# Optimization experiments

Hardware: AMD Instinct MI355X
Metric: run time of the kernel (lower is better)

The kernel has to match this reference:

```python
import jax, jax.numpy as jnp
import numpy as np


def _gru_scan(x, m, d, Wih, Whh, bih, bhh):
    # Returns pre-update hidden at each step (hiddens.append(hidden) BEFORE rnn_cell)
    H = Whh.shape[1]
    B = x.shape[0]
    h0 = jnp.zeros((B, H), x.dtype)
    xs = (jnp.swapaxes(x, 0, 1), jnp.swapaxes(m, 0, 1), jnp.swapaxes(d, 0, 1))  # [T,B,V]

    def step(h, inp):
        xt, mt, dt = inp
        gi = jnp.concatenate([xt, mt, dt], axis=1) @ Wih.T + bih  # [B,3H]
        gh = h @ Whh.T + bhh
        ir, iz, inn = jnp.split(gi, 3, axis=1)
        hr, hz, hn = jnp.split(gh, 3, axis=1)
        r = jax.nn.sigmoid(ir + hr)
        z = jax.nn.sigmoid(iz + hz)
        n = jnp.tanh(inn + r * hn)
        h_new = (1.0 - z) * n + z * h
        return h_new, h

    _, hs = jax.lax.scan(step, h0, xs)
    return jnp.swapaxes(hs, 0, 1)  # [B,T,H]


def setup_inputs() -> dict:
    key = jax.random.key(0)
    B, T, V, H = 512, 128, 59, 512
    ks = jax.random.split(key, 12)

    def u(k, shape, fan_in):
        s = 1.0 / np.sqrt(fan_in).astype(np.float32)
        return jax.random.uniform(k, shape, jnp.float32, -s, s)

    return {
        "values": jax.random.normal(ks[0], (B, T, V), jnp.float32),
        "masks": (jax.random.uniform(ks[1], (B, T, V)) < 0.8).astype(jnp.float32),
        "deltas_f": jax.random.uniform(ks[2], (B, T, V), jnp.float32),
        "deltas_b": jax.random.uniform(ks[3], (B, T, V), jnp.float32),
        # GRUCell(input=3V, hidden=H)
        "Wih": u(ks[4], (3 * H, 3 * V), 3 * V),
        "Whh": u(ks[5], (3 * H, H), H),
        "bih": jnp.zeros((3 * H,), jnp.float32),
        "bhh": jnp.zeros((3 * H,), jnp.float32),
        # hist_reg: Linear(2H -> V)
        "Wh": u(ks[6], (V, 2 * H), 2 * H),
        "bh": jnp.zeros((V,), jnp.float32),
        "Wf": u(ks[7], (V, V), V),
        "bf": jnp.zeros((V,), jnp.float32),
        # weight_combine: Linear(2V -> V)
        "Wc": u(ks[8], (V, 2 * V), 2 * V),
        "bc": jnp.zeros((V,), jnp.float32),
        # imputation: Linear(V -> V)
        "Wi": u(ks[9], (V, V), V),
        "bi": jnp.zeros((V,), jnp.float32),
    }


def reference(values, masks, deltas_f, deltas_b, Wih, Whh, bih, bhh,
              Wh, bh, Wf, bf, Wc, bc, Wi, bi):
    V = values.shape[-1]
    # forward-direction hiddens
    hf = _gru_scan(values, masks, deltas_f, Wih, Whh, bih, bhh)  # [B,T,H]
    # backward-direction: run GRU on time-flipped x/masks with deltas_b, then reverse list
    hb = _gru_scan(values[:, ::-1], masks[:, ::-1], deltas_b, Wih, Whh, bih, bhh)[:, ::-1]
    h = jnp.concatenate([hf, hb], axis=-1)  # [B,T,2H]
    x_v = h @ Wh.T + bh  # hist_reg
    mdiag = 1.0 - jnp.eye(V, dtype=values.dtype)
    x_u = values @ (Wf * mdiag).T + bf  # feat_reg
    x_h = x_u + jnp.concatenate([x_v, masks], axis=-1) @ Wc.T + bc
    imp = x_h @ Wi.T + bi
    # per-timestep masked MAE, summed over T (denominator is per-step mask count)
    num = jnp.sum(jnp.abs(values - imp) * masks, axis=(0, 2))  # [T]
    den = jnp.sum(masks, axis=(0, 2)) + 1e-5
    x_loss = jnp.sum(num / den)
    x_imp = masks * values + (1.0 - masks) * imp
    return x_imp, x_loss
```

## Files before the change

### kernel.cpp

```cpp
#include <hip/hip_runtime.h>
#include <stdint.h>


typedef unsigned short ushort_t;
typedef __bf16 bf16x8 __attribute__((ext_vector_type(8)));
typedef float f32x4 __attribute__((ext_vector_type(4)));
typedef unsigned int u32x4 __attribute__((ext_vector_type(4)));

__device__ __forceinline__ ushort_t f2bf(float f) {
    union { float f; uint32_t u; } c; c.f = f;
    uint32_t u = c.u;
    uint32_t r = (u + 0x7FFFu + ((u >> 16) & 1u)) >> 16;
    return (ushort_t)r;
}

__device__ __forceinline__ u32x4 load_b128_mall(const void* p) {
    u32x4 d;
    asm volatile("global_load_dwordx4 %0, %1, off sc0 sc1"
                 : "=v"(d) : "v"(p) : "memory");
    return d;
}
__device__ __forceinline__ void store_b16_mall(void* p, unsigned v) {
    asm volatile("global_store_short %0, %1, off sc0 sc1"
                 :: "v"(p), "v"(v) : "memory");
}

__device__ __forceinline__ float fast_sigmoid(float x) {
    float e = __expf(-x);
    return __builtin_amdgcn_rcpf(1.f + e);
}
__device__ __forceinline__ float fast_tanh(float x) {
    float xc = fminf(fmaxf(x, -15.f), 15.f);
    float e = __expf(-2.f * xc);
    return (1.f - e) * __builtin_amdgcn_rcpf(1.f + e);
}

__global__ void prep_small(const float* __restrict__ Wih, const float* __restrict__ Whh,
                           const float* __restrict__ Wh,
                           const float* __restrict__ Wf, const float* __restrict__ bf_,
                           const float* __restrict__ Wc, const float* __restrict__ bc,
                           const float* __restrict__ Wi, const float* __restrict__ bi,
                           ushort_t* __restrict__ WhhB, ushort_t* __restrict__ WihB,
                           ushort_t* __restrict__ WhpB,
                           ushort_t* __restrict__ hf0, ushort_t* __restrict__ hb0,
                           float* __restrict__ hstate,
                           ushort_t* __restrict__ Wpost1, ushort_t* __restrict__ Wpost2,
                           float* __restrict__ bcP, float* __restrict__ biP,
                           unsigned* __restrict__ bar)
{
    long long gid = (long long)blockIdx.x * blockDim.x + threadIdx.x;
    long long stride = (long long)gridDim.x * blockDim.x;

    for (long long i = gid; i < 16 * 64; i += stride) bar[i] = 0u;
    for (long long i = gid; i < 1024LL * 512; i += stride) hstate[i] = 0.f;
    for (long long i = gid; i < 512LL * 512; i += stride) { hf0[i] = 0; hb0[i] = 0; }
    for (long long i = gid; i < 1536LL * 512; i += stride) WhhB[i] = f2bf(Whh[i]);
    for (long long i = gid; i < 1536LL * 192; i += stride) {
        int n = (int)(i / 192), c = (int)(i % 192);
        WihB[i] = (c < 177) ? f2bf(Wih[n * 177 + c]) : (ushort_t)0;
    }
    for (long long i = gid; i < 64LL * 1024; i += stride) {
        int n = (int)(i >> 10), k = (int)(i & 1023);
        WhpB[i] = (n < 59) ? f2bf(Wh[n * 1024 + k]) : (ushort_t)0;
    }
    for (long long i = gid; i < 64LL * 192; i += stride) {
        int n = (int)(i / 192), c = (int)(i % 192);
        float w = 0.f;
        if (n < 59) {
            if (c < 59)       w = (c == n) ? 0.f : Wf[n * 59 + c];
            else if (c < 118) w = Wc[n * 118 + (c - 59)];
            else if (c < 177) w = Wc[n * 118 + 59 + (c - 118)];
        }
        Wpost1[i] = f2bf(w);
    }
    for (long long i = gid; i < 64LL * 64; i += stride) {
        int n = (int)(i >> 6), k = (int)(i & 63);
        Wpost2[i] = (n < 59 && k < 59) ? f2bf(Wi[n * 59 + k]) : (ushort_t)0;
    }
    for (long long i = gid; i < 64; i += stride) {
        bcP[i] = (i < 59) ? (bf_[i] + bc[i]) : 0.f;
        biP[i] = (i < 59) ? bi[i] : 0.f;
    }
}

__global__ __launch_bounds__(192)
void prep_panels(const float* __restrict__ values, const float* __restrict__ masks,
                 const float* __restrict__ deltas_f, const float* __restrict__ deltas_b,
                 ushort_t* __restrict__ xcat_f, ushort_t* __restrict__ xcat_b,
                 ushort_t* __restrict__ pcat)
{
    const int row = blockIdx.x;
    const int c = threadIdx.x;
    const int b = row >> 7, t = row & 127;
    const int tr = 127 - t;
    const long long rowr = (long long)b * 128 + tr;

    float vf = 0.f;
    if (c < 59)       vf = values  [(long long)row * 59 + c];
    else if (c < 118) vf = masks   [(long long)row * 59 + (c - 59)];
    else if (c < 177) vf = deltas_f[(long long)row * 59 + (c - 118)];
    xcat_f[((size_t)t * 512 + b) * 192 + c] = (c < 177) ? f2bf(vf) : (ushort_t)0;

    float vb = 0.f;
    if (c < 59)       vb = values  [rowr * 59 + c];
    else if (c < 118) vb = masks   [rowr * 59 + (c - 59)];
    else if (c < 177) vb = deltas_b[(long long)row * 59 + (c - 118)];
    xcat_b[((size_t)t * 512 + b) * 192 + c] = (c < 177) ? f2bf(vb) : (ushort_t)0;

    if (c < 59)
        pcat[(size_t)row * 192 + c] = f2bf(values[(long long)row * 59 + c]);
    else if (c >= 118 && c < 177)
        pcat[(size_t)row * 192 + c] = f2bf(masks[(long long)row * 59 + (c - 118)]);
    else if (c >= 177)
        pcat[(size_t)row * 192 + c] = 0;
}

__global__ __launch_bounds__(512)
void recurrence_kernel(const ushort_t* __restrict__ WhhB, const ushort_t* __restrict__ WihB,
                       const float* __restrict__ bih, const float* __restrict__ bhh,
                       const ushort_t* __restrict__ xcat_f, const ushort_t* __restrict__ xcat_b,
                       ushort_t* __restrict__ hfS, ushort_t* __restrict__ hbS,
                       unsigned* __restrict__ bar)
{
    extern __shared__ char smem_c[];
    ushort_t* Bw = (ushort_t*)smem_c;
    ushort_t* As = Bw + 96 * 704;

    const int tid  = threadIdx.x;
    const int blk  = blockIdx.x;
    const int ublk = blk & 15;
    const int mblk = blk >> 4;
    const int u0   = ublk * 32;
    const bool fwd = (mblk < 8);
    const int rbase = (fwd ? mblk : mblk - 8) * 64;
    const ushort_t* xbase = fwd ? xcat_f : xcat_b;
    ushort_t* hS = fwd ? hfS : hbS;
    unsigned* gctr = bar + (unsigned)mblk * 64;

    for (int i = tid; i < 96 * 88; i += 512) {
        int row = i / 88, q = i - row * 88;
        int g = row >> 5, u = u0 + (row & 31);
        const ushort_t* src = (q < 64)
            ? WhhB + ((size_t)(g * 512 + u)) * 512 + q * 8
            : WihB + ((size_t)(g * 512 + u)) * 192 + (q - 64) * 8;
        int qs = q ^ (row & 7);
        *(u32x4*)&Bw[row * 704 + qs * 8] = *(const u32x4*)src;
    }

    const int lane = tid & 63, wv = tid >> 6;
    const int mt = wv >> 1, tc = wv & 1;
    const int l15 = lane & 15, lhi = lane >> 4;
    const int arow = tid >> 3, aj = tid & 7;
    const int awoff = arow * 64 + ((aj ^ (arow & 7)) * 8);
    const int aSw = l15 & 7;

    const int u = u0 + tc * 16 + l15;
    const float bR  = bih[u] + bhh[u];
    const float bZ  = bih[512 + u] + bhh[512 + u];
    const float bNX = bih[1024 + u];
    const float bNH = bhh[1024 + u];

    f32x4 hreg = {0.f, 0.f, 0.f, 0.f};
    f32x4 zero = {0.f, 0.f, 0.f, 0.f};
    u32x4 r[3];

    {
        const ushort_t* xr0 = xbase + (size_t)(rbase + arow) * 192 + aj * 8;
        r[0] = load_b128_mall(xr0);
        r[1] = load_b128_mall(xr0 + 64);
        r[2] = load_b128_mall(xr0 + 128);
        asm volatile("s_waitcnt vmcnt(0)" ::: "memory");
    }
    __syncthreads();

    for (int t = 0; t < 127; ++t) {
        const ushort_t* hrow = hS + (size_t)t * 262144 + (size_t)(rbase + arow) * 512 + aj * 8;
        ushort_t* hdst = hS + (size_t)(t + 1) * 262144;

        f32x4 accR = zero, accZ = zero, accNH = zero, accNX = zero;

        *(u32x4*)&As[awoff] = r[0];
        __syncthreads();

        #pragma unroll
        for (int c = 0; c < 11; ++c) {
            if (c <= 7) r[c % 3] = load_b128_mall(hrow + c * 64);

            const ushort_t* Ab = As + (c & 1) * 4096;
            #pragma unroll
            for (int ks = 0; ks < 64; ks += 32) {
                int j  = (ks >> 3) + lhi;
                int jB = (c < 3) ? (64 + c * 8 + j) : ((c - 3) * 8 + j);
                bf16x8 a  = *(const bf16x8*)&Ab[(mt * 16 + l15) * 64 + ((j ^ aSw) * 8)];
                bf16x8 b0 = *(const bf16x8*)&Bw[( 0 + tc * 16 + l15) * 704 + ((jB ^ aSw) * 8)];
                bf16x8 b1 = *(const bf16x8*)&Bw[(32 + tc * 16 + l15) * 704 + ((jB ^ aSw) * 8)];
                bf16x8 b2 = *(const bf16x8*)&Bw[(64 + tc * 16 + l15) * 704 + ((jB ^ aSw) * 8)];
                accR = __builtin_amdgcn_mfma_f32_16x16x32_bf16(a, b0, accR, 0, 0, 0);
                accZ = __builtin_amdgcn_mfma_f32_16x16x32_bf16(a, b1, accZ, 0, 0, 0);
                if (c < 3) accNX = __builtin_amdgcn_mfma_f32_16x16x32_bf16(a, b2, accNX, 0, 0, 0);
                else       accNH = __builtin_amdgcn_mfma_f32_16x16x32_bf16(a, b2, accNH, 0, 0, 0);
            }

            if (c < 10) {
                if (c <= 7)      { asm volatile("s_waitcnt vmcnt(2)" ::: "memory"); }
                else if (c == 8) { asm volatile("s_waitcnt vmcnt(1)" ::: "memory"); }
                else             { asm volatile("s_waitcnt vmcnt(0)" ::: "memory"); }
                *(u32x4*)&As[((c + 1) & 1) * 4096 + awoff] = r[(c + 1) % 3];
                __syncthreads();
            }
        }

        #pragma unroll
        for (int reg = 0; reg < 4; ++reg) {
            int m = rbase + mt * 16 + lhi * 4 + reg;
            float rr = fast_sigmoid(accR[reg] + bR);
            float zz = fast_sigmoid(accZ[reg] + bZ);
            float nn = fast_tanh(accNX[reg] + bNX + rr * (accNH[reg] + bNH));
            float hnew = (1.f - zz) * nn + zz * hreg[reg];
            hreg[reg] = hnew;
            store_b16_mall(hdst + (size_t)m * 512 + u, (unsigned)f2bf(hnew));
        }

        if (t < 126) {
            const ushort_t* xrn = xbase + (size_t)(t + 1) * 98304
                                + (size_t)(rbase + arow) * 192 + aj * 8;
            r[0] = load_b128_mall(xrn);
            r[1] = load_b128_mall(xrn + 64);
            r[2] = load_b128_mall(xrn + 128);

            asm volatile("s_waitcnt vmcnt(0)" ::: "memory");
            __syncthreads();
            if (tid == 0) {
                atomicAdd(gctr, 1u);
                unsigned target = (unsigned)(t + 1) * 16u;
                while (__hip_atomic_load(gctr, __ATOMIC_RELAXED,
                                         __HIP_MEMORY_SCOPE_AGENT) < target)
                    __builtin_amdgcn_s_sleep(1);
            }
            __syncthreads();
        }
    }
}

__global__ __launch_bounds__(512)
void step_kernel(const ushort_t* __restrict__ hsrcF, const ushort_t* __restrict__ hsrcB,
                 ushort_t* __restrict__ hdstF, ushort_t* __restrict__ hdstB,
                 const ushort_t* __restrict__ xF, const ushort_t* __restrict__ xB,
                 const ushort_t* __restrict__ WhhB, const ushort_t* __restrict__ WihB,
                 const float* __restrict__ bih, const float* __restrict__ bhh,
                 float* __restrict__ hstate)
{
    __shared__ __align__(16) ushort_t As[64 * 64];
    __shared__ __align__(16) ushort_t Bs[96 * 64];

    const int tid  = threadIdx.x;
    const int ublk = blockIdx.x;
    const int mblk = blockIdx.y;
    const int u0   = ublk * 32;
    const bool fwd = (mblk < 8);
    const ushort_t* hsrc = fwd ? hsrcF : hsrcB;
    const ushort_t* xsrc = fwd ? xF : xB;
    ushort_t* hdst = fwd ? hdstF : hdstB;
    const int rbase = (fwd ? mblk : mblk - 8) * 64;

    const int lane = tid & 63, wv = tid >> 6;
    const int mt = wv >> 1, tc = wv & 1;
    const int l15 = lane & 15, lhi = lane >> 4;

    f32x4 zero = {0.f, 0.f, 0.f, 0.f};
    f32x4 accR = zero, accZ = zero, accNH = zero, accNX = zero;
    const int arow = tid >> 3, ac8 = (tid & 7) * 8;

    for (int chunk = 0; chunk < 11; ++chunk) {
        const bool ph1 = (chunk < 8);
        {
            const ushort_t* src = ph1
                ? hsrc + ((size_t)(rbase + arow)) * 512 + chunk * 64 + ac8
                : xsrc + ((size_t)(rbase + arow)) * 192 + (chunk - 8) * 64 + ac8;
            *(uint4*)&As[arow * 64 + ac8] = *(const uint4*)src;
        }
        {
            int rowB = tid >> 3; int c8 = (tid & 7) * 8;
            int g = rowB >> 5; int u = u0 + (rowB & 31);
            const ushort_t* src = ph1
                ? WhhB + ((size_t)(g * 512 + u)) * 512 + chunk * 64 + c8
                : WihB + ((size_t)(g * 512 + u)) * 192 + (chunk - 8) * 64 + c8;
            *(uint4*)&Bs[rowB * 64 + c8] = *(const uint4*)src;
            if (tid < 256) {
                int u2 = tid + 512;
                rowB = u2 >> 3; c8 = (u2 & 7) * 8;
                g = rowB >> 5; u = u0 + (rowB & 31);
                src = ph1
                    ? WhhB + ((size_t)(g * 512 + u)) * 512 + chunk * 64 + c8
                    : WihB + ((size_t)(g * 512 + u)) * 192 + (chunk - 8) * 64 + c8;
                *(uint4*)&Bs[rowB * 64 + c8] = *(const uint4*)src;
            }
        }
        __syncthreads();
        #pragma unroll
        for (int ks = 0; ks < 64; ks += 32) {
            bf16x8 a  = *(const bf16x8*)&As[(mt * 16 + l15) * 64 + ks + lhi * 8];
            bf16x8 b0 = *(const bf16x8*)&Bs[( 0 + tc * 16 + l15) * 64 + ks + lhi * 8];
            bf16x8 b1 = *(const bf16x8*)&Bs[(32 + tc * 16 + l15) * 64 + ks + lhi * 8];
            bf16x8 b2 = *(const bf16x8*)&Bs[(64 + tc * 16 + l15) * 64 + ks + lhi * 8];
            accR = __builtin_amdgcn_mfma_f32_16x16x32_bf16(a, b0, accR, 0, 0, 0);
            accZ = __builtin_amdgcn_mfma_f32_16x16x32_bf16(a, b1, accZ, 0, 0, 0);
            if (ph1) accNH = __builtin_amdgcn_mfma_f32_16x16x32_bf16(a, b2, accNH, 0, 0, 0);
            else     accNX = __builtin_amdgcn_mfma_f32_16x16x32_bf16(a, b2, accNX, 0, 0, 0);
        }
        __syncthreads();
    }

    const int u = u0 + tc * 16 + l15;
    const float bR  = bih[u] + bhh[u];
    const float bZ  = bih[512 + u] + bhh[512 + u];
    const float bNX = bih[1024 + u];
    const float bNH = bhh[1024 + u];
    #pragma unroll
    for (int reg = 0; reg < 4; ++reg) {
        int m = mblk * 64 + mt * 16 + lhi * 4 + reg;
        float r = 1.f / (1.f + __expf(-(accR[reg] + bR)));
        float z = 1.f / (1.f + __expf(-(accZ[reg] + bZ)));
        float n = tanhf(accNX[reg] + bNX + r * (accNH[reg] + bNH));
        size_t idx = (size_t)m * 512 + u;
        float hold = hstate[idx];
        float hnew = (1.f - z) * n + z * hold;
        hstate[idx] = hnew;
        size_t bloc = (size_t)(fwd ? m : m - 512) * 512 + u;
        hdst[bloc] = f2bf(hnew);
    }
}

__global__ __launch_bounds__(256)
void xv_kernel(const ushort_t* __restrict__ hf, const ushort_t* __restrict__ hb,
               const ushort_t* __restrict__ WhpB, const float* __restrict__ bh,
               ushort_t* __restrict__ pcat)
{
    __shared__ __align__(16) ushort_t As[128 * 64];
    __shared__ __align__(16) ushort_t Bs[64 * 64];
    const int b = blockIdx.x;
    const int tid = threadIdx.x;
    const int lane = tid & 63, wv = tid >> 6;
    const int l15 = lane & 15, lhi = lane >> 4;

    f32x4 zero = {0.f, 0.f, 0.f, 0.f};
    f32x4 acc[2][4];
    #pragma unroll
    for (int i = 0; i < 2; ++i)
        #pragma unroll
        for (int j = 0; j < 4; ++j) acc[i][j] = zero;

    for (int chunk = 0; chunk < 16; ++chunk) {
        const bool fw = (chunk < 8);
        #pragma unroll
        for (int s = 0; s < 4; ++s) {
            int unit = tid + s * 256;
            int row = unit >> 3;
            int c8 = (unit & 7) * 8;
            const ushort_t* src = fw
                ? hf + ((size_t)row * 512 + b) * 512 + chunk * 64 + c8
                : hb + ((size_t)(127 - row) * 512 + b) * 512 + (chunk - 8) * 64 + c8;
            *(uint4*)&As[row * 64 + c8] = *(const uint4*)src;
        }
        #pragma unroll
        for (int s = 0; s < 2; ++s) {
            int unit = tid + s * 256;
            int row = unit >> 3;
            int c8 = (unit & 7) * 8;
            *(uint4*)&Bs[row * 64 + c8] =
                *(const uint4*)(WhpB + (size_t)row * 1024 + chunk * 64 + c8);
        }
        __syncthreads();
        #pragma unroll
        for (int ks = 0; ks < 64; ks += 32) {
            bf16x8 bfr[4];
            #pragma unroll
            for (int nt = 0; nt < 4; ++nt)
                bfr[nt] = *(const bf16x8*)&Bs[(nt * 16 + l15) * 64 + ks + lhi * 8];
            #pragma unroll
            for (int mt2 = 0; mt2 < 2; ++mt2) {
                bf16x8 a = *(const bf16x8*)&As[(wv * 32 + mt2 * 16 + l15) * 64 + ks + lhi * 8];
                #pragma unroll
                for (int nt = 0; nt < 4; ++nt)
                    acc[mt2][nt] = __builtin_amdgcn_mfma_f32_16x16x32_bf16(a, bfr[nt], acc[mt2][nt], 0, 0, 0);
            }
        }
        __syncthreads();
    }
    #pragma unroll
    for (int mt2 = 0; mt2 < 2; ++mt2) {
        #pragma unroll
        for (int nt = 0; nt < 4; ++nt) {
            int col = nt * 16 + l15;
            if (col < 59) {
                float bhc = bh[col];
                #pragma unroll
                for (int reg = 0; reg < 4; ++reg) {
                    int t = wv * 32 + mt2 * 16 + lhi * 4 + reg;
                    pcat[((size_t)b * 128 + t) * 192 + 59 + col] = f2bf(acc[mt2][nt][reg] + bhc);
                }
            }
        }
    }
}

__global__ __launch_bounds__(256)
void post_kernel(const ushort_t* __restrict__ pcat,
                 const ushort_t* __restrict__ Wpost1, const ushort_t* __restrict__ Wpost2,
                 const float* __restrict__ bcP, const float* __restrict__ biP,
                 const float* __restrict__ values, const float* __restrict__ masks,
                 float* __restrict__ out, float* __restrict__ pnum, float* __restrict__ pden)
{
    __shared__ __align__(16) ushort_t A1[64 * 200];
    __shared__ __align__(16) ushort_t B1[64 * 200];
    __shared__ __align__(16) ushort_t B2[64 * 72];

    const int tid = threadIdx.x;
    const int blk = blockIdx.x;
    const int lane = tid & 63, wv = tid >> 6;
    const int l15 = lane & 15, lhi = lane >> 4;

    #pragma unroll
    for (int s = 0; s < 6; ++s) {
        int unit = tid + s * 256;
        int row = unit / 24, c8 = (unit % 24) * 8;
        *(uint4*)&A1[row * 200 + c8] =
            *(const uint4*)(pcat + ((size_t)blk * 64 + row) * 192 + c8);
        *(uint4*)&B1[row * 200 + c8] =
            *(const uint4*)(Wpost1 + (size_t)row * 192 + c8);
    }
    #pragma unroll
    for (int s = 0; s < 2; ++s) {
        int unit = tid + s * 256;
        int row = unit >> 3, c8 = (unit & 7) * 8;
        *(uint4*)&B2[row * 72 + c8] = *(const uint4*)(Wpost2 + (size_t)row * 64 + c8);
    }
    __syncthreads();

    f32x4 zero = {0.f, 0.f, 0.f, 0.f};
    f32x4 acc1[4];
    #pragma unroll
    for (int nt = 0; nt < 4; ++nt) acc1[nt] = zero;

    #pragma unroll
    for (int ks = 0; ks < 192; ks += 32) {
        bf16x8 a = *(const bf16x8*)&A1[(wv * 16 + l15) * 200 + ks + lhi * 8];
        #pragma unroll
        for (int nt = 0; nt < 4; ++nt) {
            bf16x8 bb = *(const bf16x8*)&B1[(nt * 16 + l15) * 200 + ks + lhi * 8];
            acc1[nt] = __builtin_amdgcn_mfma_f32_16x16x32_bf16(a, bb, acc1[nt], 0, 0, 0);
        }
    }
    __syncthreads();

    #pragma unroll
    for (int nt = 0; nt < 4; ++nt) {
        int col = nt * 16 + l15;
        float bcv = bcP[col];
        #pragma unroll
        for (int reg = 0; reg < 4; ++reg) {
            int row = wv * 16 + lhi * 4 + reg;
            A1[row * 72 + col] = f2bf(acc1[nt][reg] + bcv);
        }
    }
    __syncthreads();

    f32x4 acc2[4];
    #pragma unroll
    for (int nt = 0; nt < 4; ++nt) acc2[nt] = zero;
    #pragma unroll
    for (int ks = 0; ks < 64; ks += 32) {
        bf16x8 a = *(const bf16x8*)&A1[(wv * 16 + l15) * 72 + ks + lhi * 8];
        #pragma unroll
        for (int nt = 0; nt < 4; ++nt) {
            bf16x8 bb = *(const bf16x8*)&B2[(nt * 16 + l15) * 72 + ks + lhi * 8];
            acc2[nt] = __builtin_amdgcn_mfma_f32_16x16x32_bf16(a, bb, acc2[nt], 0, 0, 0);
        }
    }

    float biR[4];
    #pragma unroll
    for (int nt = 0; nt < 4; ++nt) biR[nt] = biP[nt * 16 + l15];

    #pragma unroll
    for (int reg = 0; reg < 4; ++reg) {
        size_t rowg = (size_t)blk * 64 + wv * 16 + lhi * 4 + reg;
        float esum = 0.f, dsum = 0.f;
        #pragma unroll
        for (int nt = 0; nt < 4; ++nt) {
            int col = nt * 16 + l15;
            if (col < 59) {
                float imp = acc2[nt][reg] + biR[nt];
                float v = values[rowg * 59 + col];
                float m = masks [rowg * 59 + col];
                out[rowg * 59 + col] = m * v + (1.f - m) * imp;
                esum += fabsf(v - imp) * m;
                dsum += m;
            }
        }
        #pragma unroll
        for (int o = 1; o < 16; o <<= 1) {
            esum += __shfl_xor(esum, o);
            dsum += __shfl_xor(dsum, o);
        }
        if (l15 == 0) { pnum[rowg] = esum; pden[rowg] = dsum; }
    }
}

__global__ __launch_bounds__(512)
void loss_kernel(const float* __restrict__ pnum, const float* __restrict__ pden,
                 float* __restrict__ out)
{
    __shared__ float sn[512], sd[512];
    int tid = threadIdx.x;
    int t = tid & 127, q = tid >> 7;
    float a = 0.f, b = 0.f;
    for (int i = 0; i < 128; ++i) {
        int bb = q * 128 + i;
        a += pnum[(size_t)bb * 128 + t];
        b += pden[(size_t)bb * 128 + t];
    }
    sn[tid] = a; sd[tid] = b;
    __syncthreads();
    if (q == 0) {
        float A = sn[t] + sn[128 + t] + sn[256 + t] + sn[384 + t];
        float B = sd[t] + sd[128 + t] + sd[256 + t] + sd[384 + t];
        sn[t] = A / (B + 1e-5f);
    }
    __syncthreads();
    if (tid == 0) {
        float s = 0.f;
        for (int i = 0; i < 128; ++i) s += sn[i];
        out[3866624] = s;
    }
}

extern "C" void kernel_launch(void* const* d_in, const int* in_sizes, int n_in,
                              void* d_out, int out_size, void* d_ws, size_t ws_size,
                              hipStream_t stream)
{
    const float* values   = (const float*)d_in[0];
    const float* masks    = (const float*)d_in[1];
    const float* deltas_f = (const float*)d_in[2];
    const float* deltas_b = (const float*)d_in[3];
    const float* Wih = (const float*)d_in[4];
    const float* Whh = (const float*)d_in[5];
    const float* bih = (const float*)d_in[6];
    const float* bhh = (const float*)d_in[7];
    const float* Wh  = (const float*)d_in[8];
    const float* bh  = (const float*)d_in[9];
    const float* Wf  = (const float*)d_in[10];
    const float* bf_ = (const float*)d_in[11];
    const float* Wc  = (const float*)d_in[12];
    const float* bc  = (const float*)d_in[13];
    const float* Wi  = (const float*)d_in[14];
    const float* bi  = (const float*)d_in[15];
    float* out = (float*)d_out;

    uint8_t* ws = (uint8_t*)d_ws;
    size_t off = 0;
    auto alloc = [&](size_t bytes) -> void* {
        void* p = ws + off;
        off = (off + bytes + 255) & ~((size_t)255);
        return p;
    };
    ushort_t* xcat_f = (ushort_t*)alloc(128ULL * 512 * 192 * 2);
    ushort_t* xcat_b = (ushort_t*)alloc(128ULL * 512 * 192 * 2);
    ushort_t* WhhB   = (ushort_t*)alloc(1536ULL * 512 * 2);
    ushort_t* WihB   = (ushort_t*)alloc(1536ULL * 192 * 2);
    ushort_t* WhpB   = (ushort_t*)alloc(64ULL * 1024 * 2);
    ushort_t* hfS    = (ushort_t*)alloc(128ULL * 512 * 512 * 2);
    ushort_t* hbS    = (ushort_t*)alloc(128ULL * 512 * 512 * 2);
    float*    hstate = (float*)alloc(1024ULL * 512 * 4);
    ushort_t* pcat   = (ushort_t*)alloc(65536ULL * 192 * 2);
    ushort_t* Wpost1 = (ushort_t*)alloc(64ULL * 192 * 2);
    ushort_t* Wpost2 = (ushort_t*)alloc(64ULL * 64 * 2);
    float*    bcP    = (float*)alloc(64 * 4);
    float*    biP    = (float*)alloc(64 * 4);
    float*    pnum   = (float*)alloc(65536ULL * 4);
    float*    pden   = (float*)alloc(65536ULL * 4);
    unsigned* bar    = (unsigned*)alloc(16 * 64 * 4);

    prep_small<<<1024, 256, 0, stream>>>(Wih, Whh, Wh, Wf, bf_, Wc, bc, Wi, bi,
                                         WhhB, WihB, WhpB, hfS, hbS, hstate,
                                         Wpost1, Wpost2, bcP, biP, bar);
    prep_panels<<<65536, 192, 0, stream>>>(values, masks, deltas_f, deltas_b,
                                           xcat_f, xcat_b, pcat);

    const unsigned smemBytes = (96u * 704u + 2u * 64u * 64u) * 2u;
    hipError_t aerr = hipFuncSetAttribute((const void*)recurrence_kernel,
                                          hipFuncAttributeMaxDynamicSharedMemorySize,
                                          (int)smemBytes);
    hipError_t lerr = hipErrorUnknown;
    if (aerr == hipSuccess) {
        const ushort_t* a0 = WhhB; const ushort_t* a1 = WihB;
        const float* a2 = bih; const float* a3 = bhh;
        const ushort_t* a4 = xcat_f; const ushort_t* a5 = xcat_b;
        ushort_t* a6 = hfS; ushort_t* a7 = hbS;
        unsigned* a8 = bar;
        void* args[] = { &a0, &a1, &a2, &a3, &a4, &a5, &a6, &a7, &a8 };
        lerr = hipLaunchCooperativeKernel((const void*)recurrence_kernel,
                                          dim3(256), dim3(512), args, smemBytes, stream);
    }
    if (lerr != hipSuccess) {
        for (int t = 0; t < 127; ++t) {
            step_kernel<<<dim3(16, 16), 512, 0, stream>>>(
                hfS + (size_t)t * 512 * 512, hbS + (size_t)t * 512 * 512,
                hfS + (size_t)(t + 1) * 512 * 512, hbS + (size_t)(t + 1) * 512 * 512,
                xcat_f + (size_t)t * 512 * 192, xcat_b + (size_t)t * 512 * 192,
                WhhB, WihB, bih, bhh, hstate);
        }
    }

    xv_kernel<<<512, 256, 0, stream>>>(hfS, hbS, WhpB, bh, pcat);
    post_kernel<<<1024, 256, 0, stream>>>(pcat, Wpost1, Wpost2, bcP, biP,
                                          values, masks, out, pnum, pden);
    loss_kernel<<<1, 512, 0, stream>>>(pnum, pden, out);
}
```

Before: 856.8 us.

## Replace atomic counter barrier with per-block step flags and direct A-fragment loads

The persistent GRU recurrence kernel no longer uses an atomic counter barrier per M-group. Each block now publishes its step number to its own flag slot, and consumers poll all 16 flags with four vector loads before reading h. The A operand no longer goes through double-buffered LDS with __syncthreads; each lane loads its x and h fragments straight from global memory. The input-projection MFMAs are issued before the wait, so they overlap the synchronisation latency. This removes per-chunk block barriers and atomic contention, but relies on global-load latency and cache coherence of the sc0 sc1 loads. prep_panels also moves to a grid-stride loop with fewer blocks.

```diff
diff --git a/kernel.cpp b/kernel.cpp
--- a/kernel.cpp
+++ b/kernel.cpp
@@ -14,15 +14,19 @@
     return (ushort_t)r;
 }
 
-__device__ __forceinline__ u32x4 load_b128_mall(const void* p) {
-    u32x4 d;
-    asm volatile("global_load_dwordx4 %0, %1, off sc0 sc1"
-                 : "=v"(d) : "v"(p) : "memory");
-    return d;
-}
 __device__ __forceinline__ void store_b16_mall(void* p, unsigned v) {
     asm volatile("global_store_short %0, %1, off sc0 sc1"
                  :: "v"(p), "v"(v) : "memory");
+}
+
+__device__ __forceinline__ void load_flags16(const unsigned* p,
+                                             u32x4& a, u32x4& b, u32x4& c, u32x4& d) {
+    asm volatile("global_load_dwordx4 %0, %4, off sc0 sc1\n\t"
+                 "global_load_dwordx4 %1, %4, off offset:16 sc0 sc1\n\t"
+                 "global_load_dwordx4 %2, %4, off offset:32 sc0 sc1\n\t"
+                 "global_load_dwordx4 %3, %4, off offset:48 sc0 sc1\n\t"
+                 "s_waitcnt vmcnt(0)"
+                 : "=v"(a), "=v"(b), "=v"(c), "=v"(d) : "v"(p) : "memory");
 }
 
 __device__ __forceinline__ float fast_sigmoid(float x) {
@@ -46,12 +50,12 @@
                            float* __restrict__ hstate,
                            ushort_t* __restrict__ Wpost1, ushort_t* __restrict__ Wpost2,
                            float* __restrict__ bcP, float* __restrict__ biP,
-                           unsigned* __restrict__ bar)
+                           unsigned* __restrict__ flags)
 {
     long long gid = (long long)blockIdx.x * blockDim.x + threadIdx.x;
     long long stride = (long long)gridDim.x * blockDim.x;
 
-    for (long long i = gid; i < 16 * 64; i += stride) bar[i] = 0u;
+    for (long long i = gid; i < 16 * 32; i += stride) flags[i] = 0u;
     for (long long i = gid; i < 1024LL * 512; i += stride) hstate[i] = 0.f;
     for (long long i = gid; i < 512LL * 512; i += stride) { hf0[i] = 0; hb0[i] = 0; }
     for (long long i = gid; i < 1536LL * 512; i += stride) WhhB[i] = f2bf(Whh[i]);
@@ -89,30 +93,42 @@
                  ushort_t* __restrict__ xcat_f, ushort_t* __restrict__ xcat_b,
                  ushort_t* __restrict__ pcat)
 {
-    const int row = blockIdx.x;
     const int c = threadIdx.x;
-    const int b = row >> 7, t = row & 127;
-    const int tr = 127 - t;
-    const long long rowr = (long long)b * 128 + tr;
-
-    float vf = 0.f;
-    if (c < 59)       vf = values  [(long long)row * 59 + c];
-    else if (c < 118) vf = masks   [(long long)row * 59 + (c - 59)];
-    else if (c < 177) vf = deltas_f[(long long)row * 59 + (c - 118)];
-    xcat_f[((size_t)t * 512 + b) * 192 + c] = (c < 177) ? f2bf(vf) : (ushort_t)0;
-
-    float vb = 0.f;
-    if (c < 59)       vb = values  [rowr * 59 + c];
-    else if (c < 118) vb = masks   [rowr * 59 + (c - 59)];
-    else if (c < 177) vb = deltas_b[(long long)row * 59 + (c - 118)];
-    xcat_b[((size_t)t * 512 + b) * 192 + c] = (c < 177) ? f2bf(vb) : (ushort_t)0;
-
-    if (c < 59)
-        pcat[(size_t)row * 192 + c] = f2bf(values[(long long)row * 59 + c]);
-    else if (c >= 118 && c < 177)
-        pcat[(size_t)row * 192 + c] = f2bf(masks[(long long)row * 59 + (c - 118)]);
-    else if (c >= 177)
-        pcat[(size_t)row * 192 + c] = 0;
+    for (int row = blockIdx.x; row < 65536; row += gridDim.x) {
+        const int b = row >> 7, t = row & 127;
+        const int tr = 127 - t;
+        const long long rowr = (long long)b * 128 + tr;
+
+        float vf = 0.f;
+        if (c < 59)       vf = values  [(long long)row * 59 + c];
+        else if (c < 118) vf = masks   [(long long)row * 59 + (c - 59)];
+        else if (c < 177) vf = deltas_f[(long long)row * 59 + (c - 118)];
+        xcat_f[((size_t)t * 512 + b) * 192 + c] = (c < 177) ? f2bf(vf) : (ushort_t)0;
+
+        float vb = 0.f;
+        if (c < 59)       vb = values  [rowr * 59 + c];
+        else if (c < 118) vb = masks   [rowr * 59 + (c - 59)];
+        else if (c < 177) vb = deltas_b[(long long)row * 59 + (c - 118)];
+        xcat_b[((size_t)t * 512 + b) * 192 + c] = (c < 177) ? f2bf(vb) : (ushort_t)0;
+
+        if (c < 59)
+            pcat[(size_t)row * 192 + c] = f2bf(values[(long long)row * 59 + c]);
+        else if (c >= 118 && c < 177)
+            pcat[(size_t)row * 192 + c] = f2bf(masks[(long long)row * 59 + (c - 118)]);
+        else if (c >= 177)
+            pcat[(size_t)row * 192 + c] = 0;
+    }
+}
+
+__device__ __forceinline__ void gates3(const ushort_t* __restrict__ Bq, int off,
+                                       bf16x8 a, f32x4& accR, f32x4& accZ, f32x4& accT)
+{
+    bf16x8 b0 = *(const bf16x8*)(Bq + off);
+    bf16x8 b1 = *(const bf16x8*)(Bq + 22528 + off);
+    bf16x8 b2 = *(const bf16x8*)(Bq + 45056 + off);
+    accR = __builtin_amdgcn_mfma_f32_16x16x32_bf16(a, b0, accR, 0, 0, 0);
+    accZ = __builtin_amdgcn_mfma_f32_16x16x32_bf16(a, b1, accZ, 0, 0, 0);
+    accT = __builtin_amdgcn_mfma_f32_16x16x32_bf16(a, b2, accT, 0, 0, 0);
 }
 
 __global__ __launch_bounds__(512)
@@ -120,11 +136,10 @@
                        const float* __restrict__ bih, const float* __restrict__ bhh,
                        const ushort_t* __restrict__ xcat_f, const ushort_t* __restrict__ xcat_b,
                        ushort_t* __restrict__ hfS, ushort_t* __restrict__ hbS,
-                       unsigned* __restrict__ bar)
+                       unsigned* __restrict__ flags)
 {
     extern __shared__ char smem_c[];
     ushort_t* Bw = (ushort_t*)smem_c;
-    ushort_t* As = Bw + 96 * 704;
 
     const int tid  = threadIdx.x;
     const int blk  = blockIdx.x;
@@ -135,7 +150,7 @@
     const int rbase = (fwd ? mblk : mblk - 8) * 64;
     const ushort_t* xbase = fwd ? xcat_f : xcat_b;
     ushort_t* hS = fwd ? hfS : hbS;
-    unsigned* gctr = bar + (unsigned)mblk * 64;
+    unsigned* gflag = flags + (unsigned)mblk * 32;
 
     for (int i = tid; i < 96 * 88; i += 512) {
         int row = i / 88, q = i - row * 88;
@@ -150,9 +165,11 @@
     const int lane = tid & 63, wv = tid >> 6;
     const int mt = wv >> 1, tc = wv & 1;
     const int l15 = lane & 15, lhi = lane >> 4;
-    const int arow = tid >> 3, aj = tid & 7;
-    const int awoff = arow * 64 + ((aj ^ (arow & 7)) * 8);
     const int aSw = l15 & 7;
+    const int arowA = mt * 16 + l15;
+
+    const ushort_t* Bq0 = Bw + (tc * 16 + l15) * 704 + ((lhi ^ aSw) * 8);
+    const ushort_t* Bq1 = Bw + (tc * 16 + l15) * 704 + (((4 + lhi) ^ aSw) * 8);
 
     const int u = u0 + tc * 16 + l15;
     const float bR  = bih[u] + bhh[u];
@@ -162,52 +179,46 @@
 
     f32x4 hreg = {0.f, 0.f, 0.f, 0.f};
     f32x4 zero = {0.f, 0.f, 0.f, 0.f};
-    u32x4 r[3];
-
-    {
-        const ushort_t* xr0 = xbase + (size_t)(rbase + arow) * 192 + aj * 8;
-        r[0] = load_b128_mall(xr0);
-        r[1] = load_b128_mall(xr0 + 64);
-        r[2] = load_b128_mall(xr0 + 128);
-        asm volatile("s_waitcnt vmcnt(0)" ::: "memory");
-    }
+
     __syncthreads();
 
     for (int t = 0; t < 127; ++t) {
-        const ushort_t* hrow = hS + (size_t)t * 262144 + (size_t)(rbase + arow) * 512 + aj * 8;
+        const ushort_t* hsrc = hS + (size_t)t * 262144;
         ushort_t* hdst = hS + (size_t)(t + 1) * 262144;
+        const ushort_t* xsrc = xbase + (size_t)t * 98304;
 
         f32x4 accR = zero, accZ = zero, accNH = zero, accNX = zero;
 
-        *(u32x4*)&As[awoff] = r[0];
-        __syncthreads();
-
-        #pragma unroll
-        for (int c = 0; c < 11; ++c) {
-            if (c <= 7) r[c % 3] = load_b128_mall(hrow + c * 64);
-
-            const ushort_t* Ab = As + (c & 1) * 4096;
-            #pragma unroll
-            for (int ks = 0; ks < 64; ks += 32) {
-                int j  = (ks >> 3) + lhi;
-                int jB = (c < 3) ? (64 + c * 8 + j) : ((c - 3) * 8 + j);
-                bf16x8 a  = *(const bf16x8*)&Ab[(mt * 16 + l15) * 64 + ((j ^ aSw) * 8)];
-                bf16x8 b0 = *(const bf16x8*)&Bw[( 0 + tc * 16 + l15) * 704 + ((jB ^ aSw) * 8)];
-                bf16x8 b1 = *(const bf16x8*)&Bw[(32 + tc * 16 + l15) * 704 + ((jB ^ aSw) * 8)];
-                bf16x8 b2 = *(const bf16x8*)&Bw[(64 + tc * 16 + l15) * 704 + ((jB ^ aSw) * 8)];
-                accR = __builtin_amdgcn_mfma_f32_16x16x32_bf16(a, b0, accR, 0, 0, 0);
-                accZ = __builtin_amdgcn_mfma_f32_16x16x32_bf16(a, b1, accZ, 0, 0, 0);
-                if (c < 3) accNX = __builtin_amdgcn_mfma_f32_16x16x32_bf16(a, b2, accNX, 0, 0, 0);
-                else       accNH = __builtin_amdgcn_mfma_f32_16x16x32_bf16(a, b2, accNH, 0, 0, 0);
+        const ushort_t* xA = xsrc + (size_t)(rbase + arowA) * 192 + lhi * 8;
+        #pragma unroll
+        for (int cx = 0; cx < 3; ++cx) {
+            bf16x8 a0 = *(const bf16x8*)(xA + cx * 64);
+            bf16x8 a1 = *(const bf16x8*)(xA + cx * 64 + 32);
+            gates3(Bq0, 512 + cx * 64, a0, accR, accZ, accNX);
+            gates3(Bq1, 512 + cx * 64, a1, accR, accZ, accNX);
+        }
+
+        {
+            const unsigned ut = (unsigned)t;
+            u32x4 fA, fB, fC, fD;
+            for (;;) {
+                load_flags16(gflag, fA, fB, fC, fD);
+                unsigned ok = (fA[0] >= ut) & (fA[1] >= ut) & (fA[2] >= ut) & (fA[3] >= ut)
+                            & (fB[0] >= ut) & (fB[1] >= ut) & (fB[2] >= ut) & (fB[3] >= ut)
+                            & (fC[0] >= ut) & (fC[1] >= ut) & (fC[2] >= ut) & (fC[3] >= ut)
+                            & (fD[0] >= ut) & (fD[1] >= ut) & (fD[2] >= ut) & (fD[3] >= ut);
+                if (ok) break;
+                __builtin_amdgcn_s_sleep(1);
             }
-
-            if (c < 10) {
-                if (c <= 7)      { asm volatile("s_waitcnt vmcnt(2)" ::: "memory"); }
-                else if (c == 8) { asm volatile("s_waitcnt vmcnt(1)" ::: "memory"); }
-                else             { asm volatile("s_waitcnt vmcnt(0)" ::: "memory"); }
-                *(u32x4*)&As[((c + 1) & 1) * 4096 + awoff] = r[(c + 1) % 3];
-                __syncthreads();
-            }
+        }
+
+        const ushort_t* hA = hsrc + (size_t)(rbase + arowA) * 512 + lhi * 8;
+        #pragma unroll
+        for (int cc = 0; cc < 8; ++cc) {
+            bf16x8 a0 = *(const bf16x8*)(hA + cc * 64);
+            bf16x8 a1 = *(const bf16x8*)(hA + cc * 64 + 32);
+            gates3(Bq0, cc * 64, a0, accR, accZ, accNH);
+            gates3(Bq1, cc * 64, a1, accR, accZ, accNH);
         }
 
         #pragma unroll
@@ -221,23 +232,12 @@
             store_b16_mall(hdst + (size_t)m * 512 + u, (unsigned)f2bf(hnew));
         }
 
-        if (t < 126) {
-            const ushort_t* xrn = xbase + (size_t)(t + 1) * 98304
-                                + (size_t)(rbase + arow) * 192 + aj * 8;
-            r[0] = load_b128_mall(xrn);
-            r[1] = load_b128_mall(xrn + 64);
-            r[2] = load_b128_mall(xrn + 128);
-
-            asm volatile("s_waitcnt vmcnt(0)" ::: "memory");
-            __syncthreads();
-            if (tid == 0) {
-                atomicAdd(gctr, 1u);
-                unsigned target = (unsigned)(t + 1) * 16u;
-                while (__hip_atomic_load(gctr, __ATOMIC_RELAXED,
-                                         __HIP_MEMORY_SCOPE_AGENT) < target)
-                    __builtin_amdgcn_s_sleep(1);
-            }
-            __syncthreads();
+        asm volatile("s_waitcnt vmcnt(0)" ::: "memory");
+        __syncthreads();
+        if (tid == 0) {
+            unsigned fv = (unsigned)(t + 1);
+            asm volatile("global_store_dword %0, %1, off sc0 sc1"
+                         :: "v"(gflag + ublk), "v"(fv) : "memory");
         }
     }
 }
@@ -579,15 +579,15 @@
     float*    biP    = (float*)alloc(64 * 4);
     float*    pnum   = (float*)alloc(65536ULL * 4);
     float*    pden   = (float*)alloc(65536ULL * 4);
-    unsigned* bar    = (unsigned*)alloc(16 * 64 * 4);
+    unsigned* flags  = (unsigned*)alloc(16 * 32 * 4);
 
     prep_small<<<1024, 256, 0, stream>>>(Wih, Whh, Wh, Wf, bf_, Wc, bc, Wi, bi,
                                          WhhB, WihB, WhpB, hfS, hbS, hstate,
-                                         Wpost1, Wpost2, bcP, biP, bar);
-    prep_panels<<<65536, 192, 0, stream>>>(values, masks, deltas_f, deltas_b,
-                                           xcat_f, xcat_b, pcat);
-
-    const unsigned smemBytes = (96u * 704u + 2u * 64u * 64u) * 2u;
+                                         Wpost1, Wpost2, bcP, biP, flags);
+    prep_panels<<<8192, 192, 0, stream>>>(values, masks, deltas_f, deltas_b,
+                                          xcat_f, xcat_b, pcat);
+
+    const unsigned smemBytes = 96u * 704u * 2u;
     hipError_t aerr = hipFuncSetAttribute((const void*)recurrence_kernel,
                                           hipFuncAttributeMaxDynamicSharedMemorySize,
                                           (int)smemBytes);
@@ -597,7 +597,7 @@
         const float* a2 = bih; const float* a3 = bhh;
         const ushort_t* a4 = xcat_f; const ushort_t* a5 = xcat_b;
         ushort_t* a6 = hfS; ushort_t* a7 = hbS;
-        unsigned* a8 = bar;
+        unsigned* a8 = flags;
         void* args[] = { &a0, &a1, &a2, &a3, &a4, &a5, &a6, &a7, &a8 };
         lerr = hipLaunchCooperativeKernel((const void*)recurrence_kernel,
                                           dim3(256), dim3(512), args, smemBytes, stream);
```

Result: slower. 1.112 ms (+29.8%).
